# Performance work log

Hardware: AMD Instinct MI355X
Metric: run time of the kernel (lower is better)

Reference implementation:

```python
import jax, jax.numpy as jnp
import numpy as np

B, N = 4, 8192


def setup_inputs() -> dict:
    key = jax.random.key(0)
    k1, k2, k3 = jax.random.split(key, 3)
    pc_pred = jax.random.normal(k1, (B, N, 3), dtype=jnp.float32)
    pc_target = jax.random.normal(k2, (B, N, 3), dtype=jnp.float32)
    fbpp = jax.random.uniform(k3, (B,), dtype=jnp.float32)
    return {"pc_pred": pc_pred, "pc_target": pc_target, "fbpp": fbpp, "lam": 1}


def _chamfer(x, y):
    # x: (B, N, 3), y: (B, M, 3)
    x2 = jnp.sum(x * x, axis=-1)                     # (B, N)
    y2 = jnp.sum(y * y, axis=-1)                     # (B, M)
    xy = jnp.einsum('bnd,bmd->bnm', x, y)            # (B, N, M)
    d2 = jnp.maximum(x2[:, :, None] + y2[:, None, :] - 2.0 * xy, 0.0)
    cham_x = jnp.mean(jnp.min(d2, axis=2), axis=1)   # (B,) pred -> target
    cham_y = jnp.mean(jnp.min(d2, axis=1), axis=1)   # (B,) target -> pred
    return jnp.mean(cham_x + cham_y)                 # scalar (batch mean)


def reference(pc_pred, pc_target, fbpp, lam):
    d = _chamfer(pc_pred, pc_target)
    r = jnp.mean(fbpp)
    return d + lam * r
```

## Files before the change

kernel.cpp:

```cpp
#include <hip/hip_runtime.h>
#include <math.h>


typedef __attribute__((ext_vector_type(8)))  short  short8;
typedef __attribute__((ext_vector_type(16))) float  f32x16;

#define YS      4
#define RPB     128
#define YTILE_T 32

static inline int roundup_h(int v, int a) { return (v + a - 1) / a * a; }

static __device__ __forceinline__ unsigned short f2bf(float f) {
    union { float f; unsigned int u; } v; v.f = f;
    unsigned int r = v.u + 0x7FFFu + ((v.u >> 16) & 1u);
    return (unsigned short)(r >> 16);
}
static __device__ __forceinline__ float bf2f(unsigned short s) {
    union { unsigned int u; float f; } v; v.u = ((unsigned int)s) << 16;
    return v.f;
}
static __device__ __forceinline__ unsigned int pk2(unsigned short lo,
                                                   unsigned short hi) {
    return (unsigned int)lo | ((unsigned int)hi << 16);
}

__global__ __launch_bounds__(256) void pack_kernel(
    const float* __restrict__ pred, const float* __restrict__ targ,
    int B, int N, int M, int NpadP, int NpadT,
    unsigned short* __restrict__ aP, unsigned short* __restrict__ bP,
    unsigned short* __restrict__ aT, unsigned short* __restrict__ bT)
{
    const int padmax = (NpadP > NpadT) ? NpadP : NpadT;
    const int gid = blockIdx.x * 256 + threadIdx.x;
    if (gid >= B * padmax) return;
    const int b = gid / padmax, i = gid - b * padmax;

    for (int cloud = 0; cloud < 2; ++cloud) {
        const int cnt  = cloud ? M : N;
        const int npad = cloud ? NpadT : NpadP;
        if (i >= npad) continue;
        const float* src = (cloud ? targ : pred) +
                           ((size_t)b * cnt + min(i, cnt - 1)) * 3;
        unsigned short* A  = (cloud ? aT : aP) + ((size_t)b * npad + i) * 16;
        unsigned short* Bk = (cloud ? bT : bP) + ((size_t)b * npad + i) * 16;

        const float xs[3] = {src[0], src[1], src[2]};
        const float n2 = xs[0]*xs[0] + xs[1]*xs[1] + xs[2]*xs[2];
        unsigned short th[3], tl[3], yh[3], yl[3];
        #pragma unroll
        for (int c = 0; c < 3; ++c) {
            const float t = -2.0f * xs[c];
            th[c] = f2bf(t);     tl[c] = f2bf(t - bf2f(th[c]));
            yh[c] = f2bf(xs[c]); yl[c] = f2bf(xs[c] - bf2f(yh[c]));
        }
        const unsigned short n2h = f2bf(n2);
        const unsigned short n2l = f2bf(n2 - bf2f(n2h));
        const unsigned short ONE = 0x3F80;

        uint4 alo, ahi, blo, bhi;
        alo.x = pk2(th[0], th[1]); alo.y = pk2(th[2], tl[0]);
        alo.z = pk2(tl[1], tl[2]); alo.w = pk2(th[0], th[1]);
        ahi.x = pk2(th[2], tl[0]); ahi.y = pk2(tl[1], tl[2]);
        ahi.z = pk2(ONE,  ONE);    ahi.w = pk2(n2h,  n2l);
        blo.x = pk2(yh[0], yh[1]); blo.y = pk2(yh[2], yh[0]);
        blo.z = pk2(yh[1], yh[2]); blo.w = pk2(yl[0], yl[1]);
        bhi.x = pk2(yl[2], yl[0]); bhi.y = pk2(yl[1], yl[2]);
        bhi.z = pk2(n2h,  n2l);    bhi.w = pk2(ONE,  ONE);

        *(uint4*)(A)      = alo;  *(uint4*)(A + 8)  = ahi;
        *(uint4*)(Bk)     = blo;  *(uint4*)(Bk + 8) = bhi;
    }
}

__global__ __launch_bounds__(256, 4) void mfma_sweep(
    const unsigned short* __restrict__ aP, const unsigned short* __restrict__ bP,
    const unsigned short* __restrict__ aT, const unsigned short* __restrict__ bT,
    int B, int N, int M, int NpadP, int NpadT, int NpadMax,
    float* __restrict__ rowpart)
{
    const int tid  = threadIdx.x;
    const int w    = tid >> 6;
    const int lane = tid & 63;
    const int lc   = lane & 31, h = lane >> 5;

    const int SP = NpadMax / RPB;
    int t = blockIdx.x;
    const int sp  = t % SP;  t /= SP;
    const int js  = t % YS;  t /= YS;
    const int b   = t % B;   t /= B;
    const int dir = t;

    const unsigned short* Xp = (dir == 0) ? aP : aT;
    const unsigned short* Yp = (dir == 0) ? bT : bP;
    const int NpadX = (dir == 0) ? NpadP : NpadT;
    const int NpadY = (dir == 0) ? NpadT : NpadP;
    const int Nx    = (dir == 0) ? N : M;
    if (sp * RPB >= NpadX) return;

    const int TM  = NpadY / 32;
    const int nt0 = (TM + YS - 1) / YS;
    const int t0  = js * nt0;
    const int nt  = min(TM - t0, nt0);
    if (nt <= 0) return;

    __shared__ unsigned short ypack[YTILE_T * 32 * 16];

    const int row0 = sp * RPB + w * 32;
    const short8 a = *reinterpret_cast<const short8*>(
        Xp + ((size_t)b * NpadX + row0 + lc) * 16 + (size_t)h * 8);

    f32x16 z, rm;
    #pragma unroll
    for (int r = 0; r < 16; ++r) { z[r] = 0.0f; rm[r] = __builtin_inff(); }
    asm("" : "+v"(z));

    for (int f0 = 0; f0 < nt; f0 += YTILE_T) {
        const int fc = min(YTILE_T, nt - f0);
        __syncthreads();
        {
            const unsigned short* src =
                Yp + ((size_t)b * NpadY + (size_t)(t0 + f0) * 32) * 16;
            const int units = fc * 64;
            for (int u = tid; u < units; u += 256) {
                const int tile = u >> 6, v = u & 63;
                const int dst  = (tile << 6) | ((v & 1) << 5) | (v >> 1);
                *(uint4*)&ypack[(size_t)dst * 8] =
                    *(const uint4*)(src + (size_t)u * 8);
            }
        }
        __syncthreads();

        int j = 0;
        for (; j + 2 <= fc; j += 2) {
            const short8 b0 = *reinterpret_cast<const short8*>(
                &ypack[(size_t)j * 512 + (size_t)lane * 8]);
            const short8 b1 = *reinterpret_cast<const short8*>(
                &ypack[(size_t)(j + 1) * 512 + (size_t)lane * 8]);
            f32x16 d0 =
                __builtin_amdgcn_mfma_f32_32x32x16_bf16(a, b0, z, 0, 0, 0);
            f32x16 d1 =
                __builtin_amdgcn_mfma_f32_32x32x16_bf16(a, b1, z, 0, 0, 0);
            asm("" : "+v"(d0), "+v"(d1));
            #pragma unroll
            for (int r = 0; r < 16; ++r)
                rm[r] = fminf(fminf(d0[r], d1[r]), rm[r]);
        }
        if (j < fc) {
            const short8 b0 = *reinterpret_cast<const short8*>(
                &ypack[(size_t)j * 512 + (size_t)lane * 8]);
            f32x16 d0 =
                __builtin_amdgcn_mfma_f32_32x32x16_bf16(a, b0, z, 0, 0, 0);
            asm("" : "+v"(d0));
            #pragma unroll
            for (int r = 0; r < 16; ++r)
                rm[r] = fminf(rm[r], d0[r]);
        }
    }

    const size_t outb = (((size_t)dir * B + b) * YS + js) * (size_t)NpadMax;
    #pragma unroll
    for (int r = 0; r < 16; ++r) {
        float v = rm[r];
        #pragma unroll
        for (int mk = 1; mk <= 16; mk <<= 1)
            v = fminf(v, __shfl_xor(v, mk, 64));
        const int row = row0 + (r & 3) + 8 * (r >> 2) + 4 * h;
        if (lc == 0 && row < Nx) rowpart[outb + row] = v;
    }
}

__global__ __launch_bounds__(256) void combine_kernel(
    const float* __restrict__ rowpart, int B, int N, int M,
    int NpadP, int NpadT, int NpadMax,
    float invBN, float invBM, float* __restrict__ partial)
{
    const int tid = threadIdx.x;
    const int tot = 2 * B * NpadMax;
    float acc = 0.f;
    for (int idx = blockIdx.x * 256 + tid; idx < tot; idx += gridDim.x * 256) {
        const int row = idx % NpadMax;
        const int rem = idx / NpadMax;
        const int b   = rem % B;
        const int dir = rem / B;
        const int Nx  = (dir == 0) ? N : M;
        if (row >= Nx) continue;
        const int NpadY = (dir == 0) ? NpadT : NpadP;
        const int TM  = NpadY / 32;
        const int nt0 = (TM + YS - 1) / YS;
        float m = __builtin_inff();
        #pragma unroll
        for (int js = 0; js < YS; ++js)
            if (js * nt0 < TM)
                m = fminf(m, rowpart[(((size_t)dir * B + b) * YS + js)
                                     * (size_t)NpadMax + row]);
        acc += fmaxf(m, 0.f) * ((dir == 0) ? invBN : invBM);
    }
    __shared__ float sb[256];
    sb[tid] = acc; __syncthreads();
    for (int off2 = 128; off2 > 0; off2 >>= 1) {
        if (tid < off2) sb[tid] += sb[tid + off2];
        __syncthreads();
    }
    if (tid == 0) partial[blockIdx.x] = sb[0];
}

__global__ void finalize_kernel(const float* __restrict__ partial, int np,
                                const float* __restrict__ fbpp, int Bf,
                                const void* __restrict__ lamp,
                                float* __restrict__ out)
{
    __shared__ float sb[256];
    const int tid = threadIdx.x;
    float acc = 0.f;
    for (int i = tid; i < np; i += 256) acc += partial[i];
    sb[tid] = acc;
    __syncthreads();
    for (int off = 128; off > 0; off >>= 1) {
        if (tid < off) sb[tid] += sb[tid + off];
        __syncthreads();
    }
    if (tid == 0) {
        const int li = *(const int*)lamp;
        const float lam = (li >= -1000000 && li <= 1000000)
                            ? (float)li : *(const float*)lamp;
        float fm = 0.f;
        for (int i = 0; i < Bf; ++i) fm += fbpp[i];
        fm /= (float)Bf;
        out[0] = sb[0] + lam * fm;
    }
}

extern "C" void kernel_launch(void* const* d_in, const int* in_sizes, int n_in,
                              void* d_out, int out_size, void* d_ws, size_t ws_size,
                              hipStream_t stream) {
    const float* pred = (const float*)d_in[0];
    const float* targ = (const float*)d_in[1];
    const float* fbpp = (const float*)d_in[2];
    const void*  lamp = d_in[3];

    const int B = in_sizes[2];
    const int N = in_sizes[0] / (3 * B);
    const int M = in_sizes[1] / (3 * B);
    const int NpadP = roundup_h(N, RPB);
    const int NpadT = roundup_h(M, RPB);
    const int NpadMax = (NpadP > NpadT) ? NpadP : NpadT;

    size_t o = 0;
    auto take = [&](size_t bytes) {
        size_t r = o; o += (bytes + 255) & ~(size_t)255; return r;
    };
    unsigned short* aP = (unsigned short*)((char*)d_ws +
                         take(((size_t)B * NpadP + 64) * 32));
    unsigned short* bP = (unsigned short*)((char*)d_ws +
                         take(((size_t)B * NpadP + 64) * 32));
    unsigned short* aT = (unsigned short*)((char*)d_ws +
                         take(((size_t)B * NpadT + 64) * 32));
    unsigned short* bT = (unsigned short*)((char*)d_ws +
                         take(((size_t)B * NpadT + 64) * 32));
    float* rowpart = (float*)((char*)d_ws +
                     take((size_t)2 * B * YS * NpadMax * sizeof(float)));
    float* partial = (float*)((char*)d_ws + take(256 * sizeof(float)));
    (void)ws_size;

    pack_kernel<<<(B * NpadMax + 255) / 256, 256, 0, stream>>>(
        pred, targ, B, N, M, NpadP, NpadT, aP, bP, aT, bT);

    const int SP = NpadMax / RPB;
    const int blocks = 2 * B * YS * SP;
    mfma_sweep<<<blocks, 256, 0, stream>>>(
        aP, bP, aT, bT, B, N, M, NpadP, NpadT, NpadMax, rowpart);

    combine_kernel<<<256, 256, 0, stream>>>(
        rowpart, B, N, M, NpadP, NpadT, NpadMax,
        1.f / ((float)B * (float)N), 1.f / ((float)B * (float)M), partial);

    finalize_kernel<<<1, 256, 0, stream>>>(partial, 256, fbpp, B, lamp,
                                           (float*)d_out);
}
```

Baseline: 44.70 us.

## Give each wave two row tiles sharing one B fragment, use DPP min-reduce

Each wave now holds two A fragments, 64 rows instead of 32, so every B fragment read from LDS feeds two MFMAs, and each block covers 256 rows. The pack kernel writes the B operand already in the lane-interleaved tile order, so the LDS staging loop becomes a straight copy with no index shuffling. The final 32-lane min reduction uses DPP and ds_swizzle in place of shfl_xor. The trade-off is more accumulator registers per wave and half as many blocks, which can lower occupancy and parallelism.

```diff
diff --git a/kernel.cpp b/kernel.cpp
--- a/kernel.cpp
+++ b/kernel.cpp
@@ -6,7 +6,7 @@
 typedef __attribute__((ext_vector_type(16))) float  f32x16;
 
 #define YS      4
-#define RPB     128
+#define RPB     256
 #define YTILE_T 32
 
 static inline int roundup_h(int v, int a) { return (v + a - 1) / a * a; }
@@ -23,6 +23,22 @@
 static __device__ __forceinline__ unsigned int pk2(unsigned short lo,
                                                    unsigned short hi) {
     return (unsigned int)lo | ((unsigned int)hi << 16);
+}
+
+static __device__ __forceinline__ float allmin32(float v) {
+    union { float f; int i; } u, t;
+    u.f = v;
+    t.i = __builtin_amdgcn_update_dpp(u.i, u.i, 0xB1, 0xF, 0xF, false);
+    u.f = fminf(u.f, t.f);
+    t.i = __builtin_amdgcn_update_dpp(u.i, u.i, 0x4E, 0xF, 0xF, false);
+    u.f = fminf(u.f, t.f);
+    t.i = __builtin_amdgcn_update_dpp(u.i, u.i, 0x124, 0xF, 0xF, false);
+    u.f = fminf(u.f, t.f);
+    t.i = __builtin_amdgcn_update_dpp(u.i, u.i, 0x128, 0xF, 0xF, false);
+    u.f = fminf(u.f, t.f);
+    t.i = __builtin_amdgcn_ds_swizzle(u.i, 0x401F);
+    u.f = fminf(u.f, t.f);
+    return u.f;
 }
 
 __global__ __launch_bounds__(256) void pack_kernel(
@@ -43,7 +59,7 @@
         const float* src = (cloud ? targ : pred) +
                            ((size_t)b * cnt + min(i, cnt - 1)) * 3;
         unsigned short* A  = (cloud ? aT : aP) + ((size_t)b * npad + i) * 16;
-        unsigned short* Bk = (cloud ? bT : bP) + ((size_t)b * npad + i) * 16;
+        unsigned short* Bk = (cloud ? bT : bP) + (size_t)b * npad * 16;
 
         const float xs[3] = {src[0], src[1], src[2]};
         const float n2 = xs[0]*xs[0] + xs[1]*xs[1] + xs[2]*xs[2];
@@ -68,8 +84,10 @@
         bhi.x = pk2(yl[2], yl[0]); bhi.y = pk2(yl[1], yl[2]);
         bhi.z = pk2(n2h,  n2l);    bhi.w = pk2(ONE,  ONE);
 
-        *(uint4*)(A)      = alo;  *(uint4*)(A + 8)  = ahi;
-        *(uint4*)(Bk)     = blo;  *(uint4*)(Bk + 8) = bhi;
+        *(uint4*)(A)     = alo;  *(uint4*)(A + 8) = ahi;
+        const size_t tb = (size_t)(i >> 5) * 64 + (i & 31);
+        *(uint4*)(Bk + tb * 8)        = blo;
+        *(uint4*)(Bk + (tb + 32) * 8) = bhi;
     }
 }
 
@@ -106,13 +124,16 @@
 
     __shared__ unsigned short ypack[YTILE_T * 32 * 16];
 
-    const int row0 = sp * RPB + w * 32;
-    const short8 a = *reinterpret_cast<const short8*>(
-        Xp + ((size_t)b * NpadX + row0 + lc) * 16 + (size_t)h * 8);
-
-    f32x16 z, rm;
+    const int row0 = sp * RPB + w * 64;
+    const size_t abase = ((size_t)b * NpadX + row0 + lc) * 16 + (size_t)h * 8;
+    const short8 a0 = *reinterpret_cast<const short8*>(Xp + abase);
+    const short8 a1 = *reinterpret_cast<const short8*>(Xp + abase + 32 * 16);
+
+    f32x16 z, rm0, rm1;
     #pragma unroll
-    for (int r = 0; r < 16; ++r) { z[r] = 0.0f; rm[r] = __builtin_inff(); }
+    for (int r = 0; r < 16; ++r) {
+        z[r] = 0.0f; rm0[r] = __builtin_inff(); rm1[r] = __builtin_inff();
+    }
     asm("" : "+v"(z));
 
     for (int f0 = 0; f0 < nt; f0 += YTILE_T) {
@@ -122,51 +143,40 @@
             const unsigned short* src =
                 Yp + ((size_t)b * NpadY + (size_t)(t0 + f0) * 32) * 16;
             const int units = fc * 64;
-            for (int u = tid; u < units; u += 256) {
-                const int tile = u >> 6, v = u & 63;
-                const int dst  = (tile << 6) | ((v & 1) << 5) | (v >> 1);
-                *(uint4*)&ypack[(size_t)dst * 8] =
+            for (int u = tid; u < units; u += 256)
+                *(uint4*)&ypack[(size_t)u * 8] =
                     *(const uint4*)(src + (size_t)u * 8);
-            }
-        }
-        __syncthreads();
-
-        int j = 0;
-        for (; j + 2 <= fc; j += 2) {
-            const short8 b0 = *reinterpret_cast<const short8*>(
+        }
+        __syncthreads();
+
+        #pragma unroll 4
+        for (int j = 0; j < fc; ++j) {
+            const short8 bq = *reinterpret_cast<const short8*>(
                 &ypack[(size_t)j * 512 + (size_t)lane * 8]);
-            const short8 b1 = *reinterpret_cast<const short8*>(
-                &ypack[(size_t)(j + 1) * 512 + (size_t)lane * 8]);
             f32x16 d0 =
-                __builtin_amdgcn_mfma_f32_32x32x16_bf16(a, b0, z, 0, 0, 0);
+                __builtin_amdgcn_mfma_f32_32x32x16_bf16(a0, bq, z, 0, 0, 0);
             f32x16 d1 =
-                __builtin_amdgcn_mfma_f32_32x32x16_bf16(a, b1, z, 0, 0, 0);
+                __builtin_amdgcn_mfma_f32_32x32x16_bf16(a1, bq, z, 0, 0, 0);
             asm("" : "+v"(d0), "+v"(d1));
             #pragma unroll
-            for (int r = 0; r < 16; ++r)
-                rm[r] = fminf(fminf(d0[r], d1[r]), rm[r]);
-        }
-        if (j < fc) {
-            const short8 b0 = *reinterpret_cast<const short8*>(
-                &ypack[(size_t)j * 512 + (size_t)lane * 8]);
-            f32x16 d0 =
-                __builtin_amdgcn_mfma_f32_32x32x16_bf16(a, b0, z, 0, 0, 0);
-            asm("" : "+v"(d0));
-            #pragma unroll
-            for (int r = 0; r < 16; ++r)
-                rm[r] = fminf(rm[r], d0[r]);
+            for (int r = 0; r < 16; ++r) {
+                rm0[r] = fminf(rm0[r], d0[r]);
+                rm1[r] = fminf(rm1[r], d1[r]);
+            }
         }
     }
 
     const size_t outb = (((size_t)dir * B + b) * YS + js) * (size_t)NpadMax;
     #pragma unroll
     for (int r = 0; r < 16; ++r) {
-        float v = rm[r];
-        #pragma unroll
-        for (int mk = 1; mk <= 16; mk <<= 1)
-            v = fminf(v, __shfl_xor(v, mk, 64));
-        const int row = row0 + (r & 3) + 8 * (r >> 2) + 4 * h;
-        if (lc == 0 && row < Nx) rowpart[outb + row] = v;
+        const float v0 = allmin32(rm0[r]);
+        const float v1 = allmin32(rm1[r]);
+        if (lc == 0) {
+            const int rr = (r & 3) + 8 * (r >> 2) + 4 * h;
+            const int ra = row0 + rr, rb = row0 + 32 + rr;
+            if (ra < Nx) rowpart[outb + ra] = v0;
+            if (rb < Nx) rowpart[outb + rb] = v1;
+        }
     }
 }
 
```

Result: slower. 73.25 us (+63.9%).
